# Performance work log

Measured on AMD Instinct MI355X. Metric: run time of the kernel, lower is better.

Reference implementation:

```python
import jax, jax.numpy as jnp
import numpy as np

B, S, HID = 1, 2048, 2048
H, KV, D = 32, 8, 64          # query heads, kv heads, head_dim
N_REP = H // KV
BASE = 10000.0


def rotate_half(x):
    x1, x2 = x[..., : D // 2], x[..., D // 2 :]
    return jnp.concatenate((-x2, x1), axis=-1)


def setup_inputs() -> dict:
    key = jax.random.key(0)
    ks = jax.random.split(key, 6)
    std = 0.02
    return {
        "hidden_states": jax.random.normal(ks[0], (B, S, HID), jnp.float32),
        "position_ids": jnp.broadcast_to(jnp.arange(S, dtype=jnp.int32), (B, S)),
        "powers": jax.random.normal(ks[1], (D // 2,), jnp.float32),
        "Wq": jax.random.normal(ks[2], (H * D, HID), jnp.float32) * std,
        "Wk": jax.random.normal(ks[3], (KV * D, HID), jnp.float32) * std,
        "Wv": jax.random.normal(ks[4], (KV * D, HID), jnp.float32) * std,
        "Wo": jax.random.normal(ks[5], (HID, H * D), jnp.float32) * std,
    }


def reference(hidden_states, position_ids, powers, Wq, Wk, Wv, Wo):
    bsz, q_len, _ = hidden_states.shape

    # QKV projections (no bias)
    q = (hidden_states @ Wq.T).reshape(bsz, q_len, H, D).transpose(0, 2, 1, 3)   # [B,H,S,D]
    k = (hidden_states @ Wk.T).reshape(bsz, q_len, KV, D).transpose(0, 2, 1, 3)  # [B,KV,S,D]
    v = (hidden_states @ Wv.T).reshape(bsz, q_len, KV, D).transpose(0, 2, 1, 3)

    # Learnable RoPE: inv_freq = base ** (-sigmoid(powers))
    inv_freq = 1.0 / (BASE ** jax.nn.sigmoid(powers))                 # [D/2]
    freqs = position_ids.astype(jnp.float32)[:, :, None] * inv_freq  # [B,S,D/2]
    emb = jnp.concatenate((freqs, freqs), axis=-1)                   # [B,S,D]
    cos = jnp.cos(emb)[:, None, :, :]                                # [B,1,S,D]
    sin = jnp.sin(emb)[:, None, :, :]

    q = q * cos + rotate_half(q) * sin
    k = k * cos + rotate_half(k) * sin

    # GQA: repeat_interleave kv heads
    k = jnp.repeat(k, N_REP, axis=1)  # [B,H,S,D]
    v = jnp.repeat(v, N_REP, axis=1)

    scores = jnp.einsum("bhqd,bhkd->bhqk", q, k) / np.sqrt(D).astype(np.float32)
    # additive causal mask (module is_causal=True)
    pos = jnp.arange(q_len)
    causal = jnp.where(pos[:, None] >= pos[None, :], 0.0, jnp.finfo(jnp.float32).min)
    scores = scores + causal

    probs = jax.nn.softmax(scores.astype(jnp.float32), axis=-1).astype(q.dtype)
    attn = jnp.einsum("bhqk,bhkd->bhqd", probs, v)                   # [B,H,S,D]
    attn = attn.transpose(0, 2, 1, 3).reshape(bsz, q_len, H * D)
    return attn @ Wo.T
```

## Files before the change

kernel.cpp:

```cpp
#include <hip/hip_runtime.h>

typedef unsigned short u16;
typedef __attribute__((ext_vector_type(8))) short short8;
typedef __attribute__((ext_vector_type(4))) short s16x4;
typedef __attribute__((ext_vector_type(4))) float f32x4;
typedef __attribute__((ext_vector_type(16))) float f32x16;
typedef __attribute__((ext_vector_type(4))) unsigned u32x4;

#define S_LEN 2048
#define HID 2048
#define NQH 32
#define NKV 8
#define HD 64
#define QKVN 3072
#define SCLOG2 0.1803368801111204f

__device__ __forceinline__ short f2b(float f){
  unsigned u = __builtin_bit_cast(unsigned, f);
  u += 0x7fffu + ((u >> 16) & 1u);
  return (short)(u >> 16);
}
__device__ __forceinline__ float b2f(u16 v){
  unsigned u = ((unsigned)v) << 16;
  return __builtin_bit_cast(float, u);
}
__device__ __forceinline__ void gll16(const void* g, void* l){
  __builtin_amdgcn_global_load_lds((const __attribute__((address_space(1))) void*)g,
                                   (__attribute__((address_space(3))) void*)l, 16, 0, 0);
}
__device__ __forceinline__ unsigned cvtpk(float a, float b){
  unsigned r;
  asm("v_cvt_pk_bf16_f32 %0, %1, %2" : "=v"(r) : "v"(a), "v"(b));
  return r;
}
__device__ __forceinline__ void pswap(unsigned &a, unsigned &b){
  asm volatile("v_permlane32_swap_b32 %0, %1" : "+v"(a), "+v"(b));
}
__device__ __forceinline__ float ex2(float x){
  float r; asm("v_exp_f32 %0, %1" : "=v"(r) : "v"(x)); return r;
}

__global__ __launch_bounds__(256) void cvt_all(const float* __restrict__ s0,
                                               const float* __restrict__ s1,
                                               const float* __restrict__ s2,
                                               const float* __restrict__ s3,
                                               const float* __restrict__ s4,
                                               u16* __restrict__ d0, u16* __restrict__ d1,
                                               u16* __restrict__ d2, u16* __restrict__ d3,
                                               u16* __restrict__ d4,
                                               const int* __restrict__ pos,
                                               const float* __restrict__ powers,
                                               float* __restrict__ cost,
                                               float* __restrict__ sint){
  int i = blockIdx.x * 256 + threadIdx.x;
  if (i >= 1835008) {
    int j = i - 1835008;
    int s = j >> 5, d = j & 31;
    float p = (float)pos[s];
    float w = powers[d];
    float sig = 1.0f / (1.0f + expf(-w));
    float inv = powf(10000.0f, -sig);
    float f = p * inv;
    cost[j] = cosf(f);
    sint[j] = sinf(f);
    return;
  }
  const float* s; u16* d; int off;
  if      (i <  524288){ s = s0; d = d0; off = i; }
  else if (i < 1048576){ s = s1; d = d1; off = i -  524288; }
  else if (i < 1179648){ s = s2; d = d2; off = i - 1048576; }
  else if (i < 1310720){ s = s3; d = d3; off = i - 1179648; }
  else                 { s = s4; d = d4; off = i - 1310720; }
  const float4* s4p = (const float4*)s;
  float4 a = s4p[off*2], b = s4p[off*2+1];
  short8 o = { f2b(a.x), f2b(a.y), f2b(a.z), f2b(a.w),
               f2b(b.x), f2b(b.y), f2b(b.z), f2b(b.w) };
  *(short8*)(d + (size_t)off*8) = o;
}

template<int MODE>
__global__ __launch_bounds__(256) void gemm_bt(const u16* __restrict__ A,
                                               const u16* __restrict__ B0,
                                               const u16* __restrict__ B1,
                                               const u16* __restrict__ B2,
                                               int n1, int n2,
                                               void* __restrict__ Cout,
                                               u16* __restrict__ vtOut,
                                               int M, int Ntot, int K,
                                               const float* __restrict__ cost,
                                               const float* __restrict__ sint){
  __shared__ alignas(16) u16 sA[2][64*64];
  __shared__ alignas(16) u16 sB[2][128*64];
  const int tid = threadIdx.x, lane = tid & 63, wv = tid >> 6;
  const int wr = wv >> 1, wc = wv & 1;
  const int m0 = blockIdx.y * 64, n0 = blockIdx.x * 128;
  const int lr = lane & 15, lg = lane >> 4;

  const u16* B;
  if (n0 < n1)      B = B0 + (size_t)n0 * K;
  else if (n0 < n2) B = B1 + (size_t)(n0 - n1) * K;
  else              B = B2 + (size_t)(n0 - n2) * K;

  const int sRow = tid >> 3;
  const int sCol = ((tid & 7) ^ (sRow & 7)) * 8;
  const u16* Arow = A + (size_t)(m0 + sRow)*K + sCol;
  const u16* Brow = B + (size_t)sRow*K + sCol;

  f32x4 acc[2][4] = {};
  const int NT = K >> 6;

  #pragma unroll
  for (int i = 0; i < 2; ++i)
    gll16(Arow + (size_t)i*32*K, (char*)&sA[0][0] + i*4096 + tid*16);
  #pragma unroll
  for (int i = 0; i < 4; ++i)
    gll16(Brow + (size_t)i*32*K, (char*)&sB[0][0] + i*4096 + tid*16);
  __syncthreads();

  for (int t = 0; t < NT; ++t) {
    const int cur = t & 1;
    if (t + 1 < NT) {
      const int kn = (t + 1) << 6;
      #pragma unroll
      for (int i = 0; i < 2; ++i)
        gll16(Arow + (size_t)i*32*K + kn, (char*)&sA[cur^1][0] + i*4096 + tid*16);
      #pragma unroll
      for (int i = 0; i < 4; ++i)
        gll16(Brow + (size_t)i*32*K + kn, (char*)&sB[cur^1][0] + i*4096 + tid*16);
    }
    const char* bA = (const char*)&sA[cur][0];
    const char* bB = (const char*)&sB[cur][0];
    #pragma unroll
    for (int kk = 0; kk < 64; kk += 32) {
      short8 af[2], bfr[4];
      #pragma unroll
      for (int m = 0; m < 2; ++m)
        af[m] = *(const short8*)(bA + (wr*32 + m*16 + lr)*128 + ((((kk>>3) + lg) ^ (lr & 7)) << 4));
      #pragma unroll
      for (int n = 0; n < 4; ++n)
        bfr[n] = *(const short8*)(bB + (wc*64 + n*16 + lr)*128 + ((((kk>>3) + lg) ^ (lr & 7)) << 4));
      #pragma unroll
      for (int m = 0; m < 2; ++m)
        #pragma unroll
        for (int n = 0; n < 4; ++n)
          acc[m][n] = __builtin_amdgcn_mfma_f32_16x16x32_bf16(af[m], bfr[n], acc[m][n], 0, 0, 0);
    }
    asm volatile("s_waitcnt vmcnt(0)" ::: "memory");
    __builtin_amdgcn_s_barrier();
  }

  if (MODE == 0 && n0 >= 2560) {
    #pragma unroll
    for (int n = 0; n < 4; ++n) {
      const int colv = n0 - 2560 + wc*64 + n*16 + lr;
      #pragma unroll
      for (int m = 0; m < 2; ++m) {
        const int row = m0 + wr*32 + m*16 + lg*4;
        s16x4 o = { f2b(acc[m][n][0]), f2b(acc[m][n][1]),
                    f2b(acc[m][n][2]), f2b(acc[m][n][3]) };
        *(s16x4*)&vtOut[(size_t)colv*S_LEN + row] = o;
      }
    }
  } else if (MODE == 0) {
    const float qsc = (n0 < n1) ? SCLOG2 : 1.0f;
    #pragma unroll
    for (int m = 0; m < 2; ++m)
      #pragma unroll
      for (int r = 0; r < 4; ++r) {
        int row = m0 + wr*32 + m*16 + lg*4 + r;
        float c0 = cost[row*32 + lr],      s0 = sint[row*32 + lr];
        float c1 = cost[row*32 + 16 + lr], s1 = sint[row*32 + 16 + lr];
        float x0 = acc[m][0][r], x1 = acc[m][1][r];
        float x2 = acc[m][2][r], x3 = acc[m][3][r];
        float o0 = (x0*c0 - x2*s0)*qsc, o2 = (x2*c0 + x0*s0)*qsc;
        float o1 = (x1*c1 - x3*s1)*qsc, o3 = (x3*c1 + x1*s1)*qsc;
        u16* cp = (u16*)Cout + (size_t)row*Ntot + n0 + wc*64 + lr;
        cp[0]  = (u16)f2b(o0);
        cp[16] = (u16)f2b(o1);
        cp[32] = (u16)f2b(o2);
        cp[48] = (u16)f2b(o3);
      }
  } else {
    #pragma unroll
    for (int m = 0; m < 2; ++m)
      #pragma unroll
      for (int n = 0; n < 4; ++n)
        #pragma unroll
        for (int r = 0; r < 4; ++r) {
          int row = m0 + wr*32 + m*16 + lg*4 + r;
          int col = n0 + wc*64 + n*16 + lr;
          ((float*)Cout)[(size_t)row*Ntot + col] = acc[m][n][r];
        }
  }
}

__global__ __launch_bounds__(256) void flash_attn(const u16* __restrict__ qkv,
                                                  const u16* __restrict__ vt,
                                                  u16* __restrict__ attn,
                                                  float* __restrict__ pO,
                                                  float* __restrict__ pL){
  __shared__ alignas(16) u16 sK[4][32*64];
  __shared__ alignas(16) u16 sVT[2][64*64];
  static const int c_tab[24] = {7,15,15,14,14,6,13,13,12,12,5,11,11,
                                10,10,4,9,9,8,8,3,2,1,0};
  static const int s_tab[24] = {2,0,1,0,1,2,0,1,0,1,2,0,1,
                                0,1,2,0,1,0,1,2,2,2,2};
  const int tid = threadIdx.x, lane = tid & 63, w = tid >> 6;
  const int h = blockIdx.x, kvh = h >> 2;
  const int chunk = c_tab[blockIdx.y];
  const int sl = s_tab[blockIdx.y];
  int t0, ntb;
  if (sl == 2) { t0 = 0; ntb = 4*chunk + 4; }
  else         { t0 = sl*2*(chunk + 1); ntb = 2*(chunk + 1); }

  const int l5 = lane & 31, hi = lane >> 5;
  const int q0w = chunk*128 + w*32;
  const int qg = q0w + l5;

  const int kRow = lane >> 3;
  const u16* srcK = qkv + (size_t)(8*w + kRow)*QKVN + HID + kvh*HD
                    + ((lane & 7) ^ (kRow & 7))*8;
  const u16* srcV = vt + (size_t)(kvh*HD + 16*w + (lane >> 3))*S_LEN
                    + ((lane & 7) ^ (lane >> 3))*8;

  auto STAGE_K = [&](int t, int buf){
    gll16(srcK + (size_t)(t*32)*QKVN, (char*)&sK[buf][0] + w*1024);
  };
  auto STAGE_V = [&](int pair, int buf){
    char* dV = (char*)&sVT[buf][0] + w*2048;
    gll16(srcV + pair*64,                    dV);
    gll16(srcV + pair*64 + (size_t)8*S_LEN,  dV + 1024);
  };

  short8 qf[4];
  #pragma unroll
  for (int cc = 0; cc < 4; ++cc)
    qf[cc] = *(const short8*)&qkv[(size_t)(q0w + l5)*QKVN + h*HD + cc*16 + hi*8];

  f32x16 accO[2] = {};
  float l_part = 0.f;

  STAGE_K(t0, 0);
  STAGE_K(t0 + 1, 1);
  STAGE_V(t0 >> 1, (t0 >> 1) & 1);

  auto QK = [&](const char* bK)->f32x16{
    short8 kf[4];
    #pragma unroll
    for (int cc = 0; cc < 4; ++cc)
      kf[cc] = *(const short8*)(bK + l5*128 + (((cc*2 + hi) ^ (l5 & 7))*16));
    __builtin_amdgcn_s_setprio(1);
    f32x16 za = {}, zb = {};
    za = __builtin_amdgcn_mfma_f32_32x32x16_bf16(kf[0], qf[0], za, 0, 0, 0);
    zb = __builtin_amdgcn_mfma_f32_32x32x16_bf16(kf[1], qf[1], zb, 0, 0, 0);
    za = __builtin_amdgcn_mfma_f32_32x32x16_bf16(kf[2], qf[2], za, 0, 0, 0);
    zb = __builtin_amdgcn_mfma_f32_32x32x16_bf16(kf[3], qf[3], zb, 0, 0, 0);
    __builtin_amdgcn_s_setprio(0);
    return za + zb;
  };

  auto SMPV = [&](int kt, int p, const char* bV, f32x16& z){
    if (kt + 31 > q0w) {
      #pragma unroll
      for (int r = 0; r < 16; ++r) {
        const int k = kt + (r&3) + 8*(r>>2) + 4*hi;
        float e = ex2(z[r]);
        z[r] = (k > qg) ? 0.f : e;
      }
    } else {
      #pragma unroll
      for (int r = 0; r < 16; ++r) z[r] = ex2(z[r]);
    }
    float s0 = (z[0]+z[1]) + (z[2]+z[3]);
    float s1 = (z[4]+z[5]) + (z[6]+z[7]);
    float s2 = (z[8]+z[9]) + (z[10]+z[11]);
    float s3 = (z[12]+z[13]) + (z[14]+z[15]);
    l_part += (s0+s1) + (s2+s3);

    short8 pa[2];
    {
      unsigned a0 = cvtpk(z[0],  z[1]);
      unsigned c0 = cvtpk(z[2],  z[3]);
      unsigned b0 = cvtpk(z[4],  z[5]);
      unsigned d0 = cvtpk(z[6],  z[7]);
      pswap(a0, b0); pswap(c0, d0);
      u32x4 w0 = {a0, c0, b0, d0};
      pa[0] = __builtin_bit_cast(short8, w0);
      unsigned a1 = cvtpk(z[8],  z[9]);
      unsigned c1 = cvtpk(z[10], z[11]);
      unsigned b1 = cvtpk(z[12], z[13]);
      unsigned d1 = cvtpk(z[14], z[15]);
      pswap(a1, b1); pswap(c1, d1);
      u32x4 w1 = {a1, c1, b1, d1};
      pa[1] = __builtin_bit_cast(short8, w1);
    }
    __builtin_amdgcn_s_setprio(1);
    #pragma unroll
    for (int s4 = 0; s4 < 2; ++s4)
      #pragma unroll
      for (int db = 0; db < 2; ++db) {
        short8 vf = *(const short8*)(bV + (db*32 + l5)*128 + (((p*4 + s4*2 + hi) ^ (l5 & 7))*16));
        accO[db] = __builtin_amdgcn_mfma_f32_32x32x16_bf16(vf, pa[s4], accO[db], 0, 0, 0);
      }
    __builtin_amdgcn_s_setprio(0);
  };

  for (int lt = 0; lt < ntb; lt += 2) {
    const int gp = (t0 + lt) >> 1;
    asm volatile("s_waitcnt vmcnt(0)" ::: "memory");
    __builtin_amdgcn_s_barrier();
    if (lt + 2 < ntb) {
      STAGE_K(t0 + lt + 2, (lt + 2) & 3);
      STAGE_K(t0 + lt + 3, (lt + 3) & 3);
      STAGE_V(gp + 1, (gp + 1) & 1);
    }

    const int ktA = (t0 + lt)*32, ktB = ktA + 32;
    const bool doA = (ktA <= q0w + 31);
    const bool doB = (ktB <= q0w + 31);
    const char* bKA = (const char*)&sK[lt & 3][0];
    const char* bKB = (const char*)&sK[(lt + 1) & 3][0];
    const char* bV  = (const char*)&sVT[gp & 1][0];

    f32x16 stA, stB;
    if (doA) stA = QK(bKA);
    if (doB) stB = QK(bKB);
    if (doA) SMPV(ktA, 0, bV, stA);
    if (doB) SMPV(ktB, 1, bV, stB);
  }

  const float l_run = l_part + __shfl_xor(l_part, 32);
  if (sl == 2) {
    const float invl = 1.0f / l_run;
    #pragma unroll
    for (int db = 0; db < 2; ++db)
      #pragma unroll
      for (int g2 = 0; g2 < 4; ++g2) {
        s16x4 o = { f2b(accO[db][g2*4+0]*invl), f2b(accO[db][g2*4+1]*invl),
                    f2b(accO[db][g2*4+2]*invl), f2b(accO[db][g2*4+3]*invl) };
        *(s16x4*)&attn[(size_t)(q0w + l5)*HID + h*HD + db*32 + g2*8 + hi*4] = o;
      }
  } else {
    const int slot = (h*8 + (chunk - 8))*2 + sl;
    const int row = w*32 + l5;
    float* po = pO + (size_t)slot*128*64 + (size_t)row*64;
    #pragma unroll
    for (int db = 0; db < 2; ++db)
      #pragma unroll
      for (int g2 = 0; g2 < 4; ++g2) {
        f32x4 v = { accO[db][g2*4+0], accO[db][g2*4+1],
                    accO[db][g2*4+2], accO[db][g2*4+3] };
        *(f32x4*)&po[db*32 + g2*8 + hi*4] = v;
      }
    if (lane < 32)
      pL[(size_t)slot*128 + row] = l_run;
  }
}

__global__ __launch_bounds__(256) void combine(const float* __restrict__ pO,
                                               const float* __restrict__ pL,
                                               u16* __restrict__ attn){
  int i = blockIdx.x * 256 + threadIdx.x;
  int d8 = i & 7;
  int row = (i >> 3) & 127;
  int cc = (i >> 10) & 7;
  int h = i >> 13;
  int slot0 = (h*8 + cc)*2;
  float l = pL[(size_t)slot0*128 + row] + pL[(size_t)(slot0+1)*128 + row];
  const float* p0 = pO + (size_t)slot0*128*64 + (size_t)row*64 + d8*8;
  const float* p1 = p0 + 128*64;
  const float inv = 1.0f / l;
  short8 o;
  #pragma unroll
  for (int j = 0; j < 8; ++j)
    o[j] = f2b((p0[j] + p1[j]) * inv);
  const int q = (8 + cc)*128 + row;
  *(short8*)&attn[(size_t)q*HID + h*HD + d8*8] = o;
}

extern "C" void kernel_launch(void* const* d_in, const int* in_sizes, int n_in,
                              void* d_out, int out_size, void* d_ws, size_t ws_size,
                              hipStream_t stream){
  const float* hs     = (const float*)d_in[0];
  const int*   pos    = (const int*)d_in[1];
  const float* powers = (const float*)d_in[2];
  const float* Wq     = (const float*)d_in[3];
  const float* Wk     = (const float*)d_in[4];
  const float* Wv     = (const float*)d_in[5];
  const float* Wo     = (const float*)d_in[6];
  float* out = (float*)d_out;

  char* ws = (char*)d_ws;
  auto take = [&](size_t bytes){ void* p = ws; ws += (bytes + 255) & ~(size_t)255; return p; };
  u16* hs_b  = (u16*)take((size_t)S_LEN*HID*2);
  u16* wq_b  = (u16*)take((size_t)HID*HID*2);
  u16* wk_b  = (u16*)take((size_t)NKV*HD*HID*2);
  u16* wv_b  = (u16*)take((size_t)NKV*HD*HID*2);
  u16* wo_b  = (u16*)take((size_t)HID*HID*2);
  u16* qkv   = (u16*)take((size_t)S_LEN*QKVN*2);
  u16* vt    = (u16*)take((size_t)NKV*HD*S_LEN*2);
  u16* attnb = (u16*)take((size_t)S_LEN*HID*2);
  float* cost = (float*)take((size_t)S_LEN*32*4);
  float* sint = (float*)take((size_t)S_LEN*32*4);
  float* pO   = (float*)take((size_t)NQH*8*2*128*64*4);
  float* pL   = (float*)take((size_t)NQH*8*2*128*4);

  cvt_all<<<7424, 256, 0, stream>>>(hs, Wq, Wk, Wv, Wo,
                                    hs_b, wq_b, wk_b, wv_b, wo_b,
                                    pos, powers, cost, sint);

  gemm_bt<0><<<dim3(QKVN/128, S_LEN/64), 256, 0, stream>>>(
      hs_b, wq_b, wk_b, wv_b, HID, HID + NKV*HD, qkv, vt,
      S_LEN, QKVN, HID, cost, sint);

  flash_attn<<<dim3(NQH, 24), 256, 0, stream>>>(qkv, vt, attnb, pO, pL);
  combine<<<1024, 256, 0, stream>>>(pO, pL, attnb);

  gemm_bt<1><<<dim3(HID/128, S_LEN/64), 256, 0, stream>>>(
      attnb, wo_b, wo_b, wo_b, 1<<28, 1<<29, out, nullptr,
      S_LEN, HID, HID, nullptr, nullptr);
}
```

Measured before the change: 116.1 us.

## Fuse split-KV combine into flash attention via last-arriver atomic counter

Removes the separate combine kernel. Each split block writes its partial output and row sums, fences, and increments a per-(head,chunk) counter, and the second block to arrive merges its sibling's partial with its own registers and writes the bf16 output. This saves one kernel launch and a reread of both partials, at the cost of an extra memset, thread fences and an atomic per split block.

```diff
diff --git a/kernel.cpp b/kernel.cpp
--- a/kernel.cpp
+++ b/kernel.cpp
@@ -198,9 +198,11 @@
                                                   const u16* __restrict__ vt,
                                                   u16* __restrict__ attn,
                                                   float* __restrict__ pO,
-                                                  float* __restrict__ pL){
+                                                  float* __restrict__ pL,
+                                                  int* __restrict__ flags){
   __shared__ alignas(16) u16 sK[4][32*64];
   __shared__ alignas(16) u16 sVT[2][64*64];
+  __shared__ int lastFlag;
   static const int c_tab[24] = {7,15,15,14,14,6,13,13,12,12,5,11,11,
                                 10,10,4,9,9,8,8,3,2,1,0};
   static const int s_tab[24] = {2,0,1,0,1,2,0,1,0,1,2,0,1,
@@ -341,7 +343,8 @@
         *(s16x4*)&attn[(size_t)(q0w + l5)*HID + h*HD + db*32 + g2*8 + hi*4] = o;
       }
   } else {
-    const int slot = (h*8 + (chunk - 8))*2 + sl;
+    const int pairIdx = h*8 + (chunk - 8);
+    const int slot = pairIdx*2 + sl;
     const int row = w*32 + l5;
     float* po = pO + (size_t)slot*128*64 + (size_t)row*64;
     #pragma unroll
@@ -354,28 +357,30 @@
       }
     if (lane < 32)
       pL[(size_t)slot*128 + row] = l_run;
+    __threadfence();
+    __syncthreads();
+    if (tid == 0)
+      lastFlag = atomicAdd(&flags[pairIdx], 1);
+    __syncthreads();
+    if (lastFlag == 1) {
+      __threadfence();
+      const int sib = slot ^ 1;
+      const float* ps = pO + (size_t)sib*128*64 + (size_t)row*64;
+      const float lsib = pL[(size_t)sib*128 + row];
+      const float invl = 1.0f / (l_run + lsib);
+      #pragma unroll
+      for (int db = 0; db < 2; ++db)
+        #pragma unroll
+        for (int g2 = 0; g2 < 4; ++g2) {
+          f32x4 sv = *(const f32x4*)&ps[db*32 + g2*8 + hi*4];
+          s16x4 o = { f2b((accO[db][g2*4+0]+sv[0])*invl),
+                      f2b((accO[db][g2*4+1]+sv[1])*invl),
+                      f2b((accO[db][g2*4+2]+sv[2])*invl),
+                      f2b((accO[db][g2*4+3]+sv[3])*invl) };
+          *(s16x4*)&attn[(size_t)(q0w + l5)*HID + h*HD + db*32 + g2*8 + hi*4] = o;
+        }
+    }
   }
-}
-
-__global__ __launch_bounds__(256) void combine(const float* __restrict__ pO,
-                                               const float* __restrict__ pL,
-                                               u16* __restrict__ attn){
-  int i = blockIdx.x * 256 + threadIdx.x;
-  int d8 = i & 7;
-  int row = (i >> 3) & 127;
-  int cc = (i >> 10) & 7;
-  int h = i >> 13;
-  int slot0 = (h*8 + cc)*2;
-  float l = pL[(size_t)slot0*128 + row] + pL[(size_t)(slot0+1)*128 + row];
-  const float* p0 = pO + (size_t)slot0*128*64 + (size_t)row*64 + d8*8;
-  const float* p1 = p0 + 128*64;
-  const float inv = 1.0f / l;
-  short8 o;
-  #pragma unroll
-  for (int j = 0; j < 8; ++j)
-    o[j] = f2b((p0[j] + p1[j]) * inv);
-  const int q = (8 + cc)*128 + row;
-  *(short8*)&attn[(size_t)q*HID + h*HD + d8*8] = o;
 }
 
 extern "C" void kernel_launch(void* const* d_in, const int* in_sizes, int n_in,
@@ -404,6 +409,9 @@
   float* sint = (float*)take((size_t)S_LEN*32*4);
   float* pO   = (float*)take((size_t)NQH*8*2*128*64*4);
   float* pL   = (float*)take((size_t)NQH*8*2*128*4);
+  int* flags  = (int*)take((size_t)NQH*8*4);
+
+  hipMemsetAsync(flags, 0, (size_t)NQH*8*4, stream);
 
   cvt_all<<<7424, 256, 0, stream>>>(hs, Wq, Wk, Wv, Wo,
                                     hs_b, wq_b, wk_b, wv_b, wo_b,
@@ -413,8 +421,7 @@
       hs_b, wq_b, wk_b, wv_b, HID, HID + NKV*HD, qkv, vt,
       S_LEN, QKVN, HID, cost, sint);
 
-  flash_attn<<<dim3(NQH, 24), 256, 0, stream>>>(qkv, vt, attnb, pO, pL);
-  combine<<<1024, 256, 0, stream>>>(pO, pL, attnb);
+  flash_attn<<<dim3(NQH, 24), 256, 0, stream>>>(qkv, vt, attnb, pO, pL, flags);
 
   gemm_bt<1><<<dim3(HID/128, S_LEN/64), 256, 0, stream>>>(
       attnb, wo_b, wo_b, wo_b, 1<<28, 1<<29, out, nullptr,
```

Measured after the change: 225.0 us. +93.7%, slower.
